# Kernel optimization log

Measured on AMD Instinct MI355X. Metric: run time of the kernel, lower is better.

The kernel has to match this reference:

```python
import jax, jax.numpy as jnp
import numpy as np

NUM_HEADS = 16  # matches init_kwargs


def _linear(x, W, b):
    # torch nn.Linear: x @ W.T + b
    return jnp.matmul(x, W.T) + b


def setup_inputs() -> dict:
    key = jax.random.key(0)
    ks = jax.random.split(key, 5)
    B, S, Dm = 8, 2048, 1024
    scale = 0.02
    return {
        "q": jax.random.normal(ks[0], (B, S, Dm), dtype=jnp.float32),
        "k": jax.random.normal(ks[1], (B, S, Dm), dtype=jnp.float32),
        "v": jax.random.normal(ks[2], (B, S, Dm), dtype=jnp.float32),
        "W": jax.random.normal(ks[3], (Dm, Dm), dtype=jnp.float32) * scale,
        "b": jax.random.normal(ks[4], (Dm,), dtype=jnp.float32) * scale,
    }


def reference(q, k, v, W, b):
    B, S, Dm = q.shape
    H = NUM_HEADS
    D = Dm // H  # head_dim

    def proj(x):
        # linear -> view(B, S, H, D) -> transpose(2, 3): (B, S, D, H)
        # NOTE: original code transposes dims 2 and 3 (head_dim <-> heads),
        # NOT the usual (1, 2); we reproduce that exactly.
        y = _linear(x, W, b).reshape(B, S, H, D)
        return jnp.swapaxes(y, 2, 3)  # (B, S, D, H)

    qh, kh, vh = proj(q), proj(k), proj(v)

    # scores: (B, S, D, H) @ (B, S, H, D) -> (B, S, D, D), scaled by sqrt(head_dim)
    logits = jnp.einsum("bsdh,bseh->bsde", qh, kh) / jnp.sqrt(jnp.float32(D))
    attn = jax.nn.softmax(logits, axis=-1)
    out = jnp.einsum("bsde,bseh->bsdh", attn, vh)  # (B, S, D, H)

    # transpose(1, 2) -> (B, D, S, H), then view(B, -1, model_dim)
    concat = jnp.swapaxes(out, 1, 2).reshape(B, -1, Dm)  # (B, S, Dm)
    return _linear(concat, W, b)
```

## Files before the change

kernel.cpp:

```cpp
#include <hip/hip_runtime.h>
#include <hip/hip_fp16.h>
#include <math.h>

typedef _Float16 f16;
typedef _Float16 half8_t __attribute__((ext_vector_type(8)));
typedef _Float16 half4_t __attribute__((ext_vector_type(4)));
typedef _Float16 half2_t __attribute__((ext_vector_type(2)));
typedef __fp16   fp16x2  __attribute__((ext_vector_type(2)));
typedef float    float4_t __attribute__((ext_vector_type(4)));

__device__ f16 Wh[1024 * 1024];

__device__ __forceinline__ void gl_lds16(const void* g, void* l) {
    __builtin_amdgcn_global_load_lds(
        (const __attribute__((address_space(1))) void*)g,
        (__attribute__((address_space(3))) void*)l,
        16, 0, 0);
}

__device__ __forceinline__ half2_t pkrtz(float a, float b) {
    fp16x2 r = __builtin_amdgcn_cvt_pkrtz(a, b);
    return __builtin_bit_cast(half2_t, r);
}

__device__ __forceinline__ half8_t cvt8(float4_t lo, float4_t hi) {
    half2_t p0 = pkrtz(lo[0], lo[1]);
    half2_t p1 = pkrtz(lo[2], lo[3]);
    half2_t p2 = pkrtz(hi[0], hi[1]);
    half2_t p3 = pkrtz(hi[2], hi[3]);
    half8_t r;
    r[0] = p0[0]; r[1] = p0[1]; r[2] = p1[0]; r[3] = p1[1];
    r[4] = p2[0]; r[5] = p2[1]; r[6] = p3[0]; r[7] = p3[1];
    return r;
}

__global__ __launch_bounds__(256) void convert_w_kernel(const float* __restrict__ W) {
    const int i = (blockIdx.x * 256 + threadIdx.x) * 8;
    const float4_t a = *(const float4_t*)(W + i);
    const float4_t b = *(const float4_t*)(W + i + 4);
    half8_t h;
#pragma unroll
    for (int t = 0; t < 4; ++t) h[t] = (f16)a[t];
#pragma unroll
    for (int t = 0; t < 4; ++t) h[4 + t] = (f16)b[t];
    *(half8_t*)(Wh + i) = h;
}


__device__ __forceinline__ void stage16(const f16* __restrict__ base, f16* dst,
                                        int tid, int kt) {
#pragma unroll
    for (int it = 0; it < 4; ++it) {
        const int ch = tid + it * 512;
        const int r = ch >> 3, s = ch & 7;
        gl_lds16(base + (size_t)r * 1024 + kt + ((s ^ (r & 7)) << 3), dst + ch * 8);
    }
}

__device__ __forceinline__ void loadA32(const float* __restrict__ base, int tid,
                                        int kt, int itbase, float4_t g[4]) {
#pragma unroll
    for (int it = 0; it < 2; ++it) {
        const int ch = tid + (itbase + it) * 512;
        const int r = ch >> 3, s = ch & 7;
        const float* p = base + (size_t)r * 1024 + kt + ((s ^ (r & 7)) << 3);
        g[2 * it]     = *(const float4_t*)p;
        g[2 * it + 1] = *(const float4_t*)(p + 4);
    }
}

__device__ __forceinline__ void writeA32(f16* dst, int tid, int itbase,
                                         const float4_t g[4]) {
#pragma unroll
    for (int it = 0; it < 2; ++it) {
        const int ch = tid + (itbase + it) * 512;
        *(half8_t*)(dst + ch * 8) = cvt8(g[2 * it], g[2 * it + 1]);
    }
}

template <typename TA, typename TC>
__device__ __forceinline__ void gemm_tile256(const TA* __restrict__ A,
                                             const float* __restrict__ bias,
                                             TC* __restrict__ C) {
    constexpr int K = 1024, N = 1024, NT = 16;
    constexpr bool AF32 = (sizeof(TA) == 4);
    __shared__ __align__(16) f16 smem[65536];
    f16* const Asb = smem;
    f16* const Bsb = smem + 32768;

    const int tid  = threadIdx.x;
    const int lane = tid & 63;
    const int wave = tid >> 6;
    const int wr   = wave >> 2;
    const int wc   = wave & 3;
    const int lrow = lane & 15;
    const int kq   = lane >> 4;
    const int row0 = blockIdx.x * 256;
    const int col0 = blockIdx.y * 256;

    const f16*   Ag16 = nullptr;
    const float* Ag32 = nullptr;
    if constexpr (AF32) Ag32 = (const float*)A + (size_t)row0 * K;
    else                Ag16 = (const f16*)A + (size_t)row0 * K;
    const f16* const Bg = Wh + (size_t)col0 * K;

    float4_t acc[8][4];
#pragma unroll
    for (int i = 0; i < 8; ++i)
#pragma unroll
        for (int j = 0; j < 4; ++j)
            acc[i][j] = (float4_t){0.f, 0.f, 0.f, 0.f};

    if constexpr (AF32) {
        stage16(Bg, Bsb, tid, 0);
        float4_t g0[4], g1[4];
        loadA32(Ag32, tid, 0, 0, g0);
        loadA32(Ag32, tid, 0, 2, g1);
        writeA32(Asb, tid, 0, g0);
        writeA32(Asb, tid, 2, g1);
        asm volatile("s_waitcnt vmcnt(0)" ::: "memory");
        asm volatile("s_waitcnt lgkmcnt(0)" ::: "memory");
    } else {
        stage16(Ag16, Asb, tid, 0);
        stage16(Bg, Bsb, tid, 0);
    }

    for (int u = 0; u < NT; ++u) {
        const int cur = u & 1;
        const f16* const Ac = Asb + (cur << 14);
        const f16* const Bc = Bsb + (cur << 14);
        f16* const An = Asb + ((cur ^ 1) << 14);
        f16* const Bn = Bsb + ((cur ^ 1) << 14);
        const int kn = ((u + 1) & (NT - 1)) * 64;

        float4_t ga0[4], ga1[4];
        if constexpr (AF32) {
            loadA32(Ag32, tid, kn, 0, ga0);
            loadA32(Ag32, tid, kn, 2, ga1);
            stage16(Bg, Bn, tid, kn);
            asm volatile("s_waitcnt vmcnt(12)" ::: "memory");
        } else {
            stage16(Ag16, An, tid, kn);
            stage16(Bg, Bn, tid, kn);
            asm volatile("s_waitcnt vmcnt(8)" ::: "memory");
        }
        __builtin_amdgcn_s_barrier();

        half8_t bfv[4][2];
#pragma unroll
        for (int j = 0; j < 4; ++j) {
            const int n = wc * 64 + j * 16 + lrow;
#pragma unroll
            for (int ks = 0; ks < 2; ++ks)
                bfv[j][ks] = *(const half8_t*)(Bc + n * 64 + (((ks * 4 + kq) ^ (n & 7)) << 3));
        }

        {
            half8_t afv[4][2];
#pragma unroll
            for (int i = 0; i < 4; ++i) {
                const int m = wr * 128 + i * 16 + lrow;
#pragma unroll
                for (int ks = 0; ks < 2; ++ks)
                    afv[i][ks] = *(const half8_t*)(Ac + m * 64 + (((ks * 4 + kq) ^ (m & 7)) << 3));
            }
            __builtin_amdgcn_s_setprio(1);
#pragma unroll
            for (int i = 0; i < 4; ++i)
#pragma unroll
                for (int j = 0; j < 4; ++j)
#pragma unroll
                    for (int ks = 0; ks < 2; ++ks)
                        acc[i][j] = __builtin_amdgcn_mfma_f32_16x16x32_f16(
                            afv[i][ks], bfv[j][ks], acc[i][j], 0, 0, 0);
            __builtin_amdgcn_s_setprio(0);
        }

        if constexpr (AF32) {
            writeA32(An, tid, 0, ga0);
        }

        {
            half8_t afv[4][2];
#pragma unroll
            for (int i = 0; i < 4; ++i) {
                const int m = wr * 128 + (4 + i) * 16 + lrow;
#pragma unroll
                for (int ks = 0; ks < 2; ++ks)
                    afv[i][ks] = *(const half8_t*)(Ac + m * 64 + (((ks * 4 + kq) ^ (m & 7)) << 3));
            }
            __builtin_amdgcn_s_setprio(1);
#pragma unroll
            for (int i = 0; i < 4; ++i)
#pragma unroll
                for (int j = 0; j < 4; ++j)
#pragma unroll
                    for (int ks = 0; ks < 2; ++ks)
                        acc[4 + i][j] = __builtin_amdgcn_mfma_f32_16x16x32_f16(
                            afv[i][ks], bfv[j][ks], acc[4 + i][j], 0, 0, 0);
            __builtin_amdgcn_s_setprio(0);
        }

        if constexpr (AF32) {
            writeA32(An, tid, 2, ga1);
        }
        asm volatile("s_waitcnt lgkmcnt(0)" ::: "memory");
        __builtin_amdgcn_s_barrier();
    }
    asm volatile("s_waitcnt vmcnt(0)" ::: "memory");

    const int ccol  = lane & 15;
    const int rbase = (lane >> 4) << 2;
#pragma unroll
    for (int j = 0; j < 4; ++j) {
        const int gcol = col0 + wc * 64 + j * 16 + ccol;
        const float bv = bias[gcol];
#pragma unroll
        for (int i = 0; i < 8; ++i) {
#pragma unroll
            for (int r = 0; r < 4; ++r) {
                const int grow = row0 + wr * 128 + i * 16 + rbase + r;
                C[(size_t)grow * N + gcol] = (TC)(acc[i][j][r] + bv);
            }
        }
    }
}

template <typename TA, typename TC>
__global__ __launch_bounds__(512, 2) void gemm_kernel(
    const TA* __restrict__ A, const float* __restrict__ bias,
    TC* __restrict__ C) {
    gemm_tile256<TA, TC>(A, bias, C);
}

__global__ __launch_bounds__(512, 2) void gemm_proj_kernel(
    const float* __restrict__ q, const float* __restrict__ k,
    const float* __restrict__ v, const float* __restrict__ bias,
    f16* __restrict__ cq, f16* __restrict__ ck, f16* __restrict__ cv) {
    const int z = blockIdx.z;
    const float* A = (z == 0) ? q : (z == 1) ? k : v;
    f16*         C = (z == 0) ? cq : (z == 1) ? ck : cv;
    gemm_tile256<float, f16>(A, bias, C);
}

__global__ __launch_bounds__(256) void attn_kernel(
    const f16* __restrict__ pq, const f16* __restrict__ pk,
    const f16* __restrict__ pv, f16* __restrict__ outp)
{
    __shared__ __align__(16) f16 Qs[4][64][24];
    __shared__ __align__(16) f16 Ks[4][64][24];
    __shared__ __align__(16) f16 Vs[4][16][72];
    __shared__ __align__(16) f16 Os[4][64][24];
    const int lane = threadIdx.x & 63;
    const int wave = threadIdx.x >> 6;
    const int p0 = blockIdx.x * 4;
    const int p = p0 + wave;
    const f16* qptr = pq + (size_t)p * 1024;
    const f16* kptr = pk + (size_t)p * 1024;
    const f16* vptr = pv + (size_t)p * 1024;

    {
        const int h  = lane >> 2;
        const int c0 = (lane & 3) << 4;
        const half8_t q0 = *(const half8_t*)(qptr + lane * 16);
        const half8_t q1 = *(const half8_t*)(qptr + lane * 16 + 8);
        const half8_t k0 = *(const half8_t*)(kptr + lane * 16);
        const half8_t k1 = *(const half8_t*)(kptr + lane * 16 + 8);
#pragma unroll
        for (int t = 0; t < 8; ++t) {
            Qs[wave][c0 + t][h]     = q0[t];
            Qs[wave][c0 + 8 + t][h] = q1[t];
            Ks[wave][c0 + t][h]     = k0[t];
            Ks[wave][c0 + 8 + t][h] = k1[t];
        }
        const half8_t v0 = *(const half8_t*)(vptr + lane * 16);
        const half8_t v1 = *(const half8_t*)(vptr + lane * 16 + 8);
        *(half8_t*)&Vs[wave][h][c0]     = v0;
        *(half8_t*)&Vs[wave][h][c0 + 8] = v1;
    }
    __syncthreads();

    const int g  = lane >> 4;
    const int lc = lane & 15;

    half4_t ka[4], qb[4];
#pragma unroll
    for (int t = 0; t < 4; ++t) {
        ka[t] = *(const half4_t*)&Ks[wave][16 * t + lc][4 * g];
        qb[t] = *(const half4_t*)&Qs[wave][16 * t + lc][4 * g];
    }
    float4_t s[4][4];
#pragma unroll
    for (int et = 0; et < 4; ++et)
#pragma unroll
        for (int dt = 0; dt < 4; ++dt)
            s[et][dt] = __builtin_amdgcn_mfma_f32_16x16x16f16(
                ka[et], qb[dt], (float4_t){0.f, 0.f, 0.f, 0.f}, 0, 0, 0);

    float inv[4];
#pragma unroll
    for (int dt = 0; dt < 4; ++dt) {
        float m = s[0][dt][0];
#pragma unroll
        for (int et = 0; et < 4; ++et)
#pragma unroll
            for (int r = 0; r < 4; ++r) m = fmaxf(m, s[et][dt][r]);
        m = fmaxf(m, __shfl_xor(m, 16));
        m = fmaxf(m, __shfl_xor(m, 32));
        float sum = 0.f;
#pragma unroll
        for (int et = 0; et < 4; ++et)
#pragma unroll
            for (int r = 0; r < 4; ++r) {
                const float t = __expf((s[et][dt][r] - m) * 0.125f);
                s[et][dt][r] = t;
                sum += t;
            }
        sum += __shfl_xor(sum, 16);
        sum += __shfl_xor(sum, 32);
        inv[dt] = 1.f / sum;
    }

    half4_t pa[4][4];
#pragma unroll
    for (int kt = 0; kt < 4; ++kt)
#pragma unroll
        for (int dt = 0; dt < 4; ++dt) {
            const half2_t lo = pkrtz(s[kt][dt][0] * inv[dt], s[kt][dt][1] * inv[dt]);
            const half2_t hi = pkrtz(s[kt][dt][2] * inv[dt], s[kt][dt][3] * inv[dt]);
            half4_t f;
            f[0] = lo[0]; f[1] = lo[1]; f[2] = hi[0]; f[3] = hi[1];
            pa[kt][dt] = f;
        }

    float4_t o[4];
#pragma unroll
    for (int dt = 0; dt < 4; ++dt) o[dt] = (float4_t){0.f, 0.f, 0.f, 0.f};
#pragma unroll
    for (int kt = 0; kt < 4; ++kt) {
        const half4_t vb = *(const half4_t*)&Vs[wave][lc][16 * kt + 4 * g];
#pragma unroll
        for (int dt = 0; dt < 4; ++dt)
            o[dt] = __builtin_amdgcn_mfma_f32_16x16x16f16(pa[kt][dt], vb, o[dt], 0, 0, 0);
    }

#pragma unroll
    for (int dt = 0; dt < 4; ++dt)
#pragma unroll
        for (int r = 0; r < 4; ++r)
            Os[wave][16 * dt + 4 * g + r][lc] = (f16)o[dt][r];
    __syncthreads();

    const int b0 = p0 >> 11;
    const int s0 = p0 & 2047;
#pragma unroll
    for (int hf = 0; hf < 2; ++hf) {
        const int u  = threadIdx.x + hf * 256;
        const int d  = u >> 3;
        const int si = (u >> 1) & 3;
        const int uh = u & 1;
        const half8_t val = *(const half8_t*)&Os[si][d][uh * 8];
        f16* dst = outp + ((size_t)(b0 * 64 + d) * 2048 + (s0 + si)) * 16 + uh * 8;
        *(half8_t*)dst = val;
    }
}

extern "C" void kernel_launch(void* const* d_in, const int* in_sizes, int n_in,
                              void* d_out, int out_size, void* d_ws, size_t ws_size,
                              hipStream_t stream)
{
    const float* q    = (const float*)d_in[0];
    const float* k    = (const float*)d_in[1];
    const float* v    = (const float*)d_in[2];
    const float* W    = (const float*)d_in[3];
    const float* bias = (const float*)d_in[4];
    float* out = (float*)d_out;

    const int M = 16384;
    const size_t elems = (size_t)M * 1024;

    f16* projq = (f16*)d_ws;
    f16* attn  = projq + elems;
    f16* projk = (f16*)d_out;
    f16* projv = projk + elems;

    convert_w_kernel<<<512, 256, 0, stream>>>(W);

    dim3 gridp(M / 256, 1024 / 256, 3);
    gemm_proj_kernel<<<gridp, 512, 0, stream>>>(q, k, v, bias, projq, projk, projv);
    attn_kernel<<<M / 4, 256, 0, stream>>>(projq, projk, projv, attn);
    dim3 gridf(M / 256, 1024 / 256);
    gemm_kernel<f16, float><<<gridf, 512, 0, stream>>>(attn, bias, out);
}
```

Baseline: 463.4 us.

## Pre-convert q/k/v to fp16 in a separate pass and remap GEMM block order

Adds a standalone kernel that converts the fp32 q, k and v inputs to fp16 in a global scratch buffer. The projection GEMM can then use the same direct global-to-LDS fp16 staging as the final GEMM, instead of loading fp32 into registers and converting inside the main loop. Both GEMMs also remap block indices so consecutive blocks are spread across XCD-sized groups, with the aim of improving L2 reuse of A and W tiles. The cost is an extra full read of the fp32 inputs and a 96 MB fp16 write plus re-read, in exchange for a simpler, lower-register GEMM pipeline.

After: 446.4 us. 1.04x faster.

```diff
diff --git a/kernel.cpp b/kernel.cpp
--- a/kernel.cpp
+++ b/kernel.cpp
@@ -10,6 +10,7 @@
 typedef float    float4_t __attribute__((ext_vector_type(4)));
 
 __device__ f16 Wh[1024 * 1024];
+__device__ f16 Xh[3ul * 16777216];
 
 __device__ __forceinline__ void gl_lds16(const void* g, void* l) {
     __builtin_amdgcn_global_load_lds(
@@ -46,6 +47,19 @@
     *(half8_t*)(Wh + i) = h;
 }
 
+__global__ __launch_bounds__(256) void convert_x_kernel(
+    const float* __restrict__ q, const float* __restrict__ k,
+    const float* __restrict__ v)
+{
+    const int z = blockIdx.z;
+    const float* src = (z == 0) ? q : (z == 1) ? k : v;
+    f16* dst = Xh + (size_t)z * 16777216;
+    const size_t i = ((size_t)blockIdx.x * 256 + threadIdx.x) * 8;
+    const float4_t a = *(const float4_t*)(src + i);
+    const float4_t b = *(const float4_t*)(src + i + 4);
+    *(half8_t*)(dst + i) = cvt8(a, b);
+}
+
 
 __device__ __forceinline__ void stage16(const f16* __restrict__ base, f16* dst,
                                         int tid, int kt) {
@@ -57,33 +71,12 @@
     }
 }
 
-__device__ __forceinline__ void loadA32(const float* __restrict__ base, int tid,
-                                        int kt, int itbase, float4_t g[4]) {
-#pragma unroll
-    for (int it = 0; it < 2; ++it) {
-        const int ch = tid + (itbase + it) * 512;
-        const int r = ch >> 3, s = ch & 7;
-        const float* p = base + (size_t)r * 1024 + kt + ((s ^ (r & 7)) << 3);
-        g[2 * it]     = *(const float4_t*)p;
-        g[2 * it + 1] = *(const float4_t*)(p + 4);
-    }
-}
-
-__device__ __forceinline__ void writeA32(f16* dst, int tid, int itbase,
-                                         const float4_t g[4]) {
-#pragma unroll
-    for (int it = 0; it < 2; ++it) {
-        const int ch = tid + (itbase + it) * 512;
-        *(half8_t*)(dst + ch * 8) = cvt8(g[2 * it], g[2 * it + 1]);
-    }
-}
-
-template <typename TA, typename TC>
-__device__ __forceinline__ void gemm_tile256(const TA* __restrict__ A,
+template <typename TC>
+__device__ __forceinline__ void gemm_tile256(const f16* __restrict__ A,
                                              const float* __restrict__ bias,
-                                             TC* __restrict__ C) {
+                                             TC* __restrict__ C,
+                                             int row0, int col0) {
     constexpr int K = 1024, N = 1024, NT = 16;
-    constexpr bool AF32 = (sizeof(TA) == 4);
     __shared__ __align__(16) f16 smem[65536];
     f16* const Asb = smem;
     f16* const Bsb = smem + 32768;
@@ -95,13 +88,8 @@
     const int wc   = wave & 3;
     const int lrow = lane & 15;
     const int kq   = lane >> 4;
-    const int row0 = blockIdx.x * 256;
-    const int col0 = blockIdx.y * 256;
-
-    const f16*   Ag16 = nullptr;
-    const float* Ag32 = nullptr;
-    if constexpr (AF32) Ag32 = (const float*)A + (size_t)row0 * K;
-    else                Ag16 = (const f16*)A + (size_t)row0 * K;
+
+    const f16* const Ag = A + (size_t)row0 * K;
     const f16* const Bg = Wh + (size_t)col0 * K;
 
     float4_t acc[8][4];
@@ -111,19 +99,8 @@
         for (int j = 0; j < 4; ++j)
             acc[i][j] = (float4_t){0.f, 0.f, 0.f, 0.f};
 
-    if constexpr (AF32) {
-        stage16(Bg, Bsb, tid, 0);
-        float4_t g0[4], g1[4];
-        loadA32(Ag32, tid, 0, 0, g0);
-        loadA32(Ag32, tid, 0, 2, g1);
-        writeA32(Asb, tid, 0, g0);
-        writeA32(Asb, tid, 2, g1);
-        asm volatile("s_waitcnt vmcnt(0)" ::: "memory");
-        asm volatile("s_waitcnt lgkmcnt(0)" ::: "memory");
-    } else {
-        stage16(Ag16, Asb, tid, 0);
-        stage16(Bg, Bsb, tid, 0);
-    }
+    stage16(Ag, Asb, tid, 0);
+    stage16(Bg, Bsb, tid, 0);
 
     for (int u = 0; u < NT; ++u) {
         const int cur = u & 1;
@@ -133,17 +110,9 @@
         f16* const Bn = Bsb + ((cur ^ 1) << 14);
         const int kn = ((u + 1) & (NT - 1)) * 64;
 
-        float4_t ga0[4], ga1[4];
-        if constexpr (AF32) {
-            loadA32(Ag32, tid, kn, 0, ga0);
-            loadA32(Ag32, tid, kn, 2, ga1);
-            stage16(Bg, Bn, tid, kn);
-            asm volatile("s_waitcnt vmcnt(12)" ::: "memory");
-        } else {
-            stage16(Ag16, An, tid, kn);
-            stage16(Bg, Bn, tid, kn);
-            asm volatile("s_waitcnt vmcnt(8)" ::: "memory");
-        }
+        stage16(Ag, An, tid, kn);
+        stage16(Bg, Bn, tid, kn);
+        asm volatile("s_waitcnt vmcnt(8)" ::: "memory");
         __builtin_amdgcn_s_barrier();
 
         half8_t bfv[4][2];
@@ -176,10 +145,6 @@
             __builtin_amdgcn_s_setprio(0);
         }
 
-        if constexpr (AF32) {
-            writeA32(An, tid, 0, ga0);
-        }
-
         {
             half8_t afv[4][2];
 #pragma unroll
@@ -201,9 +166,6 @@
             __builtin_amdgcn_s_setprio(0);
         }
 
-        if constexpr (AF32) {
-            writeA32(An, tid, 2, ga1);
-        }
         asm volatile("s_waitcnt lgkmcnt(0)" ::: "memory");
         __builtin_amdgcn_s_barrier();
     }
@@ -226,21 +188,23 @@
     }
 }
 
-template <typename TA, typename TC>
+template <typename TC>
 __global__ __launch_bounds__(512, 2) void gemm_kernel(
-    const TA* __restrict__ A, const float* __restrict__ bias,
+    const f16* __restrict__ A, const float* __restrict__ bias,
     TC* __restrict__ C) {
-    gemm_tile256<TA, TC>(A, bias, C);
+    const int f    = blockIdx.x + 64 * blockIdx.y;
+    const int virt = (f & 7) * 32 + (f >> 3);
+    gemm_tile256<TC>(A, bias, C, ((virt >> 2) & 63) * 256, (virt & 3) * 256);
 }
 
 __global__ __launch_bounds__(512, 2) void gemm_proj_kernel(
-    const float* __restrict__ q, const float* __restrict__ k,
-    const float* __restrict__ v, const float* __restrict__ bias,
+    const float* __restrict__ bias,
     f16* __restrict__ cq, f16* __restrict__ ck, f16* __restrict__ cv) {
-    const int z = blockIdx.z;
-    const float* A = (z == 0) ? q : (z == 1) ? k : v;
-    f16*         C = (z == 0) ? cq : (z == 1) ? ck : cv;
-    gemm_tile256<float, f16>(A, bias, C);
+    const int f    = blockIdx.x + 64 * (blockIdx.y + 4 * blockIdx.z);
+    const int virt = (f & 7) * 96 + (f >> 3);
+    const int y = virt & 3, x = (virt >> 2) & 63, z = virt >> 8;
+    f16* C = (z == 0) ? cq : (z == 1) ? ck : cv;
+    gemm_tile256<f16>(Xh + (size_t)z * 16777216, bias, C, x * 256, y * 256);
 }
 
 __global__ __launch_bounds__(256) void attn_kernel(
@@ -385,10 +349,12 @@
     f16* projv = projk + elems;
 
     convert_w_kernel<<<512, 256, 0, stream>>>(W);
+    dim3 gridc(8192, 1, 3);
+    convert_x_kernel<<<gridc, 256, 0, stream>>>(q, k, v);
 
     dim3 gridp(M / 256, 1024 / 256, 3);
-    gemm_proj_kernel<<<gridp, 512, 0, stream>>>(q, k, v, bias, projq, projk, projv);
+    gemm_proj_kernel<<<gridp, 512, 0, stream>>>(bias, projq, projk, projv);
     attn_kernel<<<M / 4, 256, 0, stream>>>(projq, projk, projv, attn);
     dim3 gridf(M / 256, 1024 / 256);
-    gemm_kernel<f16, float><<<gridf, 512, 0, stream>>>(attn, bias, out);
-}
+    gemm_kernel<float><<<gridf, 512, 0, stream>>>(attn, bias, out);
+}
```
